# Kernel tuning notes

Measured on AMD Instinct MI355X. Metric: run time of the kernel, lower is better.

Reference implementation:

```python
import jax, jax.numpy as jnp
import numpy as np

H = 16        # num_heads
D_HEAD = 128  # head_dim
D = H * D_HEAD  # hidden_size = 2048


def setup_inputs() -> dict:
    key = jax.random.key(0)
    ks = jax.random.split(key, 9)
    s = 1.0 / np.sqrt(D)
    x = jax.random.normal(ks[0], (2, 2048, D), dtype=jnp.float32)
    Wq = jax.random.uniform(ks[1], (D, D), jnp.float32, -s, s)
    bq = jax.random.uniform(ks[2], (D,), jnp.float32, -s, s)
    Wk = jax.random.uniform(ks[3], (D, D), jnp.float32, -s, s)
    bk = jax.random.uniform(ks[4], (D,), jnp.float32, -s, s)
    Wv = jax.random.uniform(ks[5], (D, D), jnp.float32, -s, s)
    bv = jax.random.uniform(ks[6], (D,), jnp.float32, -s, s)
    Wo = jax.random.uniform(ks[7], (D, D), jnp.float32, -s, s)
    bo = jax.random.uniform(ks[8], (D,), jnp.float32, -s, s)
    return {"x": x, "Wq": Wq, "bq": bq, "Wk": Wk, "bk": bk,
            "Wv": Wv, "bv": bv, "Wo": Wo, "bo": bo}


def reference(x, Wq, bq, Wk, bk, Wv, bv, Wo, bo):
    B, T, _ = x.shape
    # Linear projections (torch Linear: x @ W.T + b)
    Q = x @ Wq.T + bq
    K = x @ Wk.T + bk
    V = x @ Wv.T + bv
    # [B, T, H, Dh] -> [B, H, T, Dh]
    Q = Q.reshape(B, T, H, D_HEAD).transpose(0, 2, 1, 3)
    K = K.reshape(B, T, H, D_HEAD).transpose(0, 2, 1, 3)
    V = V.reshape(B, T, H, D_HEAD).transpose(0, 2, 1, 3)
    scores = jnp.einsum('bhqd,bhkd->bhqk', Q, K) / jnp.sqrt(jnp.float32(D_HEAD))
    causal = jnp.tril(jnp.ones((T, T), dtype=bool))
    scores = jnp.where(causal, scores, -jnp.inf)
    probs = jax.nn.softmax(scores, axis=-1)
    ctx = jnp.einsum('bhqk,bhkd->bhqd', probs, V)  # [B, H, T, Dh]
    merged = ctx.transpose(0, 2, 1, 3).reshape(B, T, D)
    return merged @ Wo.T + bo
```

## Files before the change

### kernel.cpp

```cpp
#include <hip/hip_runtime.h>
#include <hip/hip_bf16.h>
#include <math.h>

typedef unsigned short ushort_t;
typedef short bf16x8 __attribute__((ext_vector_type(8)));
typedef float f32x4 __attribute__((ext_vector_type(4)));
typedef float f32x16 __attribute__((ext_vector_type(16)));

#define NH 16
#define DH 128
#define DM 2048
#define TSEQ 2048
#define BT 4096

__device__ __forceinline__ void async16(const void* g, void* l) {
  __builtin_amdgcn_global_load_lds(
      (const __attribute__((address_space(1))) void*)g,
      (__attribute__((address_space(3))) void*)l, 16, 0, 0);
}

__device__ __forceinline__ f32x4 mfma16(bf16x8 a, bf16x8 b, f32x4 c) {
  return __builtin_amdgcn_mfma_f32_16x16x32_bf16(a, b, c, 0, 0, 0);
}
__device__ __forceinline__ f32x16 mfma32(bf16x8 a, bf16x8 b, f32x16 c) {
  return __builtin_amdgcn_mfma_f32_32x32x16_bf16(a, b, c, 0, 0, 0);
}

__device__ __forceinline__ ushort_t f2bf(float f) {
  __hip_bfloat16 h = __float2bfloat16(f);
  return *reinterpret_cast<ushort_t*>(&h);
}
__device__ __forceinline__ unsigned cvtpk_bf16(float lo, float hi_) {
  unsigned r;
  asm("v_cvt_pk_bf16_f32 %0, %1, %2" : "=v"(r) : "v"(lo), "v"(hi_));
  return r;
}
__device__ __forceinline__ float fexp2(float x) {
  float r; asm("v_exp_f32 %0, %1" : "=v"(r) : "v"(x)); return r;
}

__global__ void cvt_kernel(const float* __restrict__ in, ushort_t* __restrict__ out, int n4) {
  const int i = blockIdx.x * blockDim.x + threadIdx.x;
  if (i >= n4) return;
  const float4 v = reinterpret_cast<const float4*>(in)[i];
  ushort4 u;
  u.x = f2bf(v.x); u.y = f2bf(v.y); u.z = f2bf(v.z); u.w = f2bf(v.w);
  reinterpret_cast<ushort4*>(out)[i] = u;
}

template<int MODE>
__global__ __launch_bounds__(256)
void gemm_kernel(const ushort_t* __restrict__ A,
                 const ushort_t* __restrict__ W_0, const ushort_t* __restrict__ W_1,
                 const ushort_t* __restrict__ W_2,
                 const float* __restrict__ b_0, const float* __restrict__ b_1,
                 const float* __restrict__ b_2,
                 ushort_t* __restrict__ outQ, ushort_t* __restrict__ outK,
                 ushort_t* __restrict__ outVt, float* __restrict__ outF)
{
  constexpr int K = DM;
  __shared__ __attribute__((aligned(16))) ushort_t As[128 * 64];
  __shared__ __attribute__((aligned(16))) ushort_t Bs[128 * 64];

  const int z = (MODE == 0) ? blockIdx.z : 0;
  const ushort_t* Wp = (MODE == 0) ? (z == 0 ? W_0 : (z == 1 ? W_1 : W_2)) : W_0;
  const float* bias  = (MODE == 0) ? (z == 0 ? b_0 : (z == 1 ? b_1 : b_2)) : b_0;

  const int n0 = blockIdx.x * 128;
  const int m0 = blockIdx.y * 128;
  const int tid = threadIdx.x;
  const int w = tid >> 6, l = tid & 63;
  const int wm = w >> 1, wn = w & 1;
  const int l15 = l & 15, l4 = l >> 4;

  f32x4 zero = {0.f, 0.f, 0.f, 0.f};
  f32x4 acc[4][4];
#pragma unroll
  for (int i = 0; i < 4; ++i)
#pragma unroll
    for (int j = 0; j < 4; ++j) acc[i][j] = zero;

  for (int k0 = 0; k0 < K; k0 += 64) {
    __syncthreads();
#pragma unroll
    for (int i = 0; i < 4; ++i) {
      const int rb = (i * 4 + w) * 8;
      const int r = rb + (l >> 3);
      const int c = ((l & 7) * 8) ^ ((r & 7) * 8);
      async16(A  + (size_t)(m0 + r) * K + k0 + c, &As[rb * 64]);
      async16(Wp + (size_t)(n0 + r) * K + k0 + c, &Bs[rb * 64]);
    }
    __syncthreads();
#pragma unroll
    for (int ks = 0; ks < 2; ++ks) {
      bf16x8 af[4], bfr[4];
#pragma unroll
      for (int mf = 0; mf < 4; ++mf) {
        const int row = wm * 64 + mf * 16 + l15;
        const int byte_ = row * 128 + ((l4 * 16 + ks * 64) ^ ((row & 7) << 4));
        af[mf] = *reinterpret_cast<const bf16x8*>(reinterpret_cast<const char*>(As) + byte_);
      }
#pragma unroll
      for (int nf = 0; nf < 4; ++nf) {
        const int row = wn * 64 + nf * 16 + l15;
        const int byte_ = row * 128 + ((l4 * 16 + ks * 64) ^ ((row & 7) << 4));
        bfr[nf] = *reinterpret_cast<const bf16x8*>(reinterpret_cast<const char*>(Bs) + byte_);
      }
#pragma unroll
      for (int mf = 0; mf < 4; ++mf)
#pragma unroll
        for (int nf = 0; nf < 4; ++nf)
          acc[mf][nf] = mfma16(af[mf], bfr[nf], acc[mf][nf]);
    }
  }

#pragma unroll
  for (int nf = 0; nf < 4; ++nf) {
    const int n = n0 + wn * 64 + nf * 16 + l15;
    const float bv = bias[n];
#pragma unroll
    for (int mf = 0; mf < 4; ++mf) {
#pragma unroll
      for (int r = 0; r < 4; ++r) {
        const int m = m0 + wm * 64 + mf * 16 + l4 * 4 + r;
        const float v = acc[mf][nf][r] + bv;
        if (MODE == 1) {
          outF[(size_t)m * DM + n] = v;
        } else {
          const int b = m >> 11, t = m & 2047;
          const int hh = n >> 7, d = n & 127;
          const ushort_t val = f2bf(v);
          if (z == 2) {
            outVt[((size_t)(b * NH + hh) * DH + d) * TSEQ + t] = val;
          } else {
            ushort_t* dst = (z == 0) ? outQ : outK;
            dst[((size_t)(b * NH + hh) * TSEQ + t) * DH + d] = val;
          }
        }
      }
    }
  }
}

__device__ __forceinline__ void stage_kv(const ushort_t* __restrict__ Kg,
                                         const ushort_t* __restrict__ Vt,
                                         size_t kbase, size_t vbase, int kv0,
                                         ushort_t* KsB, ushort_t* VsB, int tid)
{
#pragma unroll
  for (int i = 0; i < 4; ++i) {
    const int idx = i * 256 + tid;
    const int r = idx >> 4, ch = idx & 15;
    const int c = (ch ^ (r & 7)) * 8;
    async16(Kg + kbase + (size_t)(kv0 + r) * DH + c, KsB + idx * 8);
  }
#pragma unroll
  for (int i = 0; i < 4; ++i) {
    const int idx = i * 256 + tid;
    const int d = idx >> 3, ch = idx & 7;
    const int c = (ch ^ (d & 7)) * 8;
    async16(Vt + vbase + (size_t)d * TSEQ + kv0 + c, VsB + idx * 8);
  }
}

__global__ __launch_bounds__(256)
void attn_kernel(const ushort_t* __restrict__ Q, const ushort_t* __restrict__ Kg,
                 const ushort_t* __restrict__ Vt, ushort_t* __restrict__ ctx)
{
  __shared__ __attribute__((aligned(16))) ushort_t Ks[2][64 * 128];
  __shared__ __attribute__((aligned(16))) ushort_t Vs[2][128 * 64];

  const int fid = (int)blockIdx.x + 16 * (int)blockIdx.y;
  const int xcd = fid & 7;
  const int s   = fid >> 3;
  const int bh  = xcd * 4 + (s & 3);
  const int qt  = (s < 32) ? (15 - (s >> 2)) : ((s - 32) >> 2);

  const int tid = threadIdx.x, w = tid >> 6, l = tid & 63;
  const int l31 = l & 31, hi = l >> 5;
  const size_t kbase = (size_t)bh * TSEQ * DH;
  const size_t vbase = (size_t)bh * DH * TSEQ;
  const int bq0 = qt * 128;
  const int wq0 = bq0 + w * 32;
  const int NT = qt * 2 + 2;
  const int q = wq0 + l31;
  const float C2 = 0.12753842f;
  const float NEG = -3.0e38f;

  bf16x8 aq[8];
  {
    const ushort_t* qp = Q + kbase + (size_t)q * DH + hi * 8;
#pragma unroll
    for (int st = 0; st < 8; ++st)
      aq[st] = *reinterpret_cast<const bf16x8*>(qp + st * 16);
  }

  f32x16 o[4] = {};
  float m_r = NEG, l_r = 0.f;

  stage_kv(Kg, Vt, kbase, vbase, 0, Ks[0], Vs[0], tid);

  for (int kt = 0; kt < NT; ++kt) {
    const int kv0 = kt * 64, cur = kt & 1;
    if (kt + 1 < NT) {
      stage_kv(Kg, Vt, kbase, vbase, kv0 + 64, Ks[cur ^ 1], Vs[cur ^ 1], tid);
      asm volatile("s_waitcnt vmcnt(8)" ::: "memory");
    } else {
      asm volatile("s_waitcnt vmcnt(0)" ::: "memory");
    }
    __builtin_amdgcn_s_barrier();

    if (kv0 <= wq0 + 31) {
      const char* ksb = reinterpret_cast<const char*>(Ks[cur]);
      f32x16 s0 = {}, s1 = {};
      __builtin_amdgcn_s_setprio(1);
#pragma unroll
      for (int st = 0; st < 8; ++st) {
        const int byt = l31 * 256 + ((hi * 16 + st * 32) ^ ((l31 & 7) << 4));
        bf16x8 ak0 = *reinterpret_cast<const bf16x8*>(ksb + byt);
        bf16x8 ak1 = *reinterpret_cast<const bf16x8*>(ksb + byt + 8192);
        s0 = mfma32(ak0, aq[st], s0);
        s1 = mfma32(ak1, aq[st], s1);
      }
      __builtin_amdgcn_s_setprio(0);

      if (kv0 + 63 > wq0) {
#pragma unroll
        for (int r = 0; r < 16; ++r) {
          const int kvl = kv0 + (r & 3) + 8 * (r >> 2) + 4 * hi;
          if (kvl > q)      s0[r] = NEG;
          if (kvl + 32 > q) s1[r] = NEG;
        }
      }

      float t8[8];
#pragma unroll
      for (int r = 0; r < 8; ++r)
        t8[r] = fmaxf(fmaxf(s0[r], s0[r + 8]), fmaxf(s1[r], s1[r + 8]));
#pragma unroll
      for (int r = 0; r < 4; ++r) t8[r] = fmaxf(t8[r], t8[r + 4]);
      float mt = fmaxf(fmaxf(t8[0], t8[1]), fmaxf(t8[2], t8[3]));
      mt = fmaxf(mt, __shfl_xor(mt, 32));

      const float mnew = fmaxf(m_r, mt);
      if (!__all(mt <= m_r + 16.0f)) {
        const float alpha = fexp2((m_r - mnew) * C2);
        l_r *= alpha;
#pragma unroll
        for (int d0 = 0; d0 < 4; ++d0) o[d0] *= alpha;
        m_r = mnew;
      }

#pragma unroll
      for (int r = 0; r < 16; ++r) {
        s0[r] = fexp2((s0[r] - m_r) * C2);
        s1[r] = fexp2((s1[r] - m_r) * C2);
      }
      float sm[8];
#pragma unroll
      for (int r = 0; r < 8; ++r) sm[r] = (s0[r] + s0[r + 8]) + (s1[r] + s1[r + 8]);
#pragma unroll
      for (int r = 0; r < 4; ++r) sm[r] += sm[r + 4];
      float ls = (sm[0] + sm[1]) + (sm[2] + sm[3]);
      ls += __shfl_xor(ls, 32);
      l_r += ls;

      const char* vsb = reinterpret_cast<const char*>(Vs[cur]);
#pragma unroll
      for (int ks = 0; ks < 4; ++ks) {
        float pj[8];
#pragma unroll
        for (int j = 0; j < 8; ++j)
          pj[j] = (ks >> 1) ? s1[(ks & 1) * 8 + j] : s0[(ks & 1) * 8 + j];
        unsigned cA = cvtpk_bf16(pj[0], pj[1]);
        unsigned cB = cvtpk_bf16(pj[2], pj[3]);
        unsigned cC = cvtpk_bf16(pj[4], pj[5]);
        unsigned cD = cvtpk_bf16(pj[6], pj[7]);
        asm volatile("v_permlane32_swap_b32 %0, %1" : "+v"(cA), "+v"(cC));
        asm volatile("v_permlane32_swap_b32 %0, %1" : "+v"(cB), "+v"(cD));
        union { unsigned u[4]; bf16x8 v; } pa;
        pa.u[0] = cA; pa.u[1] = cB; pa.u[2] = cC; pa.u[3] = cD;
        __builtin_amdgcn_s_setprio(1);
#pragma unroll
        for (int d0 = 0; d0 < 4; ++d0) {
          const int byt = (d0 * 32 + l31) * 128 + ((ks * 32 + hi * 16) ^ ((l31 & 7) << 4));
          bf16x8 av = *reinterpret_cast<const bf16x8*>(vsb + byt);
          o[d0] = mfma32(av, pa.v, o[d0]);
        }
        __builtin_amdgcn_s_setprio(0);
      }
    }
    asm volatile("" ::: "memory");
    __builtin_amdgcn_s_barrier();
  }

  const size_t obase = (size_t)(bh >> 4) * TSEQ * DM + (size_t)(bh & 15) * DH;
  const float inv = 1.0f / l_r;
  ushort_t* cp = ctx + obase + (size_t)q * DM + hi * 4;
#pragma unroll
  for (int d0 = 0; d0 < 4; ++d0) {
#pragma unroll
    for (int g = 0; g < 4; ++g) {
      ushort4 u;
      u.x = f2bf(o[d0][4 * g + 0] * inv);
      u.y = f2bf(o[d0][4 * g + 1] * inv);
      u.z = f2bf(o[d0][4 * g + 2] * inv);
      u.w = f2bf(o[d0][4 * g + 3] * inv);
      *reinterpret_cast<ushort4*>(cp + d0 * 32 + 8 * g) = u;
    }
  }
}

extern "C" void kernel_launch(void* const* d_in, const int* in_sizes, int n_in,
                              void* d_out, int out_size, void* d_ws, size_t ws_size,
                              hipStream_t stream) {
  const float* x  = (const float*)d_in[0];
  const float* Wq = (const float*)d_in[1];
  const float* bq = (const float*)d_in[2];
  const float* Wk = (const float*)d_in[3];
  const float* bk = (const float*)d_in[4];
  const float* Wv = (const float*)d_in[5];
  const float* bv = (const float*)d_in[6];
  const float* Wo = (const float*)d_in[7];
  const float* bo = (const float*)d_in[8];
  float* out = (float*)d_out;

  char* ws = (char*)d_ws;
  ushort_t* xb  = (ushort_t*)ws;  ws += (size_t)BT * DM * 2;
  ushort_t* Wqb = (ushort_t*)ws;  ws += (size_t)DM * DM * 2;
  ushort_t* Wkb = (ushort_t*)ws;  ws += (size_t)DM * DM * 2;
  ushort_t* Wvb = (ushort_t*)ws;  ws += (size_t)DM * DM * 2;
  ushort_t* Wob = (ushort_t*)ws;  ws += (size_t)DM * DM * 2;
  ushort_t* Qb  = (ushort_t*)ws;  ws += (size_t)BT * DM * 2;
  ushort_t* Kb  = (ushort_t*)ws;  ws += (size_t)BT * DM * 2;
  ushort_t* Vtb = (ushort_t*)ws;  ws += (size_t)BT * DM * 2;
  ushort_t* ctxb = xb;

  const int nx4 = BT * DM / 4, nw4 = DM * DM / 4;
  cvt_kernel<<<nx4 / 256, 256, 0, stream>>>(x,  xb,  nx4);
  cvt_kernel<<<nw4 / 256, 256, 0, stream>>>(Wq, Wqb, nw4);
  cvt_kernel<<<nw4 / 256, 256, 0, stream>>>(Wk, Wkb, nw4);
  cvt_kernel<<<nw4 / 256, 256, 0, stream>>>(Wv, Wvb, nw4);
  cvt_kernel<<<nw4 / 256, 256, 0, stream>>>(Wo, Wob, nw4);

  gemm_kernel<0><<<dim3(DM / 128, BT / 128, 3), 256, 0, stream>>>(
      xb, Wqb, Wkb, Wvb, bq, bk, bv, Qb, Kb, Vtb, nullptr);

  attn_kernel<<<dim3(TSEQ / 128, 32), 256, 0, stream>>>(Qb, Kb, Vtb, ctxb);

  gemm_kernel<1><<<dim3(DM / 128, BT / 128, 1), 256, 0, stream>>>(
      ctxb, Wob, nullptr, nullptr, bo, nullptr, nullptr,
      nullptr, nullptr, nullptr, out);
}
```

Baseline: 298.9 us.

## Replace 128x128 GEMM with double-buffered 256x256 tiles and XCD-aware block mapping

The projection GEMMs move from 128x128 tiles with 4 waves and a single-buffered LDS stage to 256x256 tiles with 8 waves. K-tiles are double-buffered in four quarter stages, with explicit vmcnt waits and barriers so the next tile's global-to-LDS loads overlap MFMA work on the current one. Block indices are remapped so neighbouring tiles land on the same XCD to improve L2 reuse, and MFMA sections are wrapped in s_setprio. The cost is much larger LDS use (128KB per block), more register pressure, and fragile hand-tuned wait counts.

```diff
diff --git a/kernel.cpp b/kernel.cpp
--- a/kernel.cpp
+++ b/kernel.cpp
@@ -48,82 +48,145 @@
   reinterpret_cast<ushort4*>(out)[i] = u;
 }
 
+__device__ __forceinline__ void stage_half_g(const ushort_t* __restrict__ src,
+                                             int row0, int k0,
+                                             ushort_t* dst, int tid) {
+#pragma unroll
+  for (int i = 0; i < 2; ++i) {
+    const int idx = i * 512 + tid;
+    const int r = idx >> 3, ch = idx & 7;
+    const int c = (ch ^ (r & 7)) * 8;
+    async16(src + (size_t)(row0 + r) * DM + k0 + c, dst + idx * 8);
+  }
+}
+
 template<int MODE>
-__global__ __launch_bounds__(256)
-void gemm_kernel(const ushort_t* __restrict__ A,
-                 const ushort_t* __restrict__ W_0, const ushort_t* __restrict__ W_1,
-                 const ushort_t* __restrict__ W_2,
-                 const float* __restrict__ b_0, const float* __restrict__ b_1,
-                 const float* __restrict__ b_2,
-                 ushort_t* __restrict__ outQ, ushort_t* __restrict__ outK,
-                 ushort_t* __restrict__ outVt, float* __restrict__ outF)
+__global__ __launch_bounds__(512, 2)
+void gemm256_kernel(const ushort_t* __restrict__ A,
+                    const ushort_t* __restrict__ W_0, const ushort_t* __restrict__ W_1,
+                    const ushort_t* __restrict__ W_2,
+                    const float* __restrict__ b_0, const float* __restrict__ b_1,
+                    const float* __restrict__ b_2,
+                    ushort_t* __restrict__ outQ, ushort_t* __restrict__ outK,
+                    ushort_t* __restrict__ outVt, float* __restrict__ outF)
 {
-  constexpr int K = DM;
-  __shared__ __attribute__((aligned(16))) ushort_t As[128 * 64];
-  __shared__ __attribute__((aligned(16))) ushort_t Bs[128 * 64];
+  constexpr int NK = DM / 64;
+  __shared__ __attribute__((aligned(16))) ushort_t As[2][2][128 * 64];
+  __shared__ __attribute__((aligned(16))) ushort_t Bs[2][2][128 * 64];
 
   const int z = (MODE == 0) ? blockIdx.z : 0;
   const ushort_t* Wp = (MODE == 0) ? (z == 0 ? W_0 : (z == 1 ? W_1 : W_2)) : W_0;
   const float* bias  = (MODE == 0) ? (z == 0 ? b_0 : (z == 1 ? b_1 : b_2)) : b_0;
 
-  const int n0 = blockIdx.x * 128;
-  const int m0 = blockIdx.y * 128;
+  const int fid = (int)blockIdx.x + 8 * (int)blockIdx.y;
+  const int xcd = fid & 7, pos = fid >> 3;
+  const int n0 = ((xcd & 1) * 4 + (pos & 3)) * 256;
+  const int m0 = ((xcd >> 1) * 4 + (pos >> 2)) * 256;
+
   const int tid = threadIdx.x;
   const int w = tid >> 6, l = tid & 63;
-  const int wm = w >> 1, wn = w & 1;
+  const int wr = w >> 2, wc = w & 3;
   const int l15 = l & 15, l4 = l >> 4;
 
-  f32x4 zero = {0.f, 0.f, 0.f, 0.f};
-  f32x4 acc[4][4];
-#pragma unroll
-  for (int i = 0; i < 4; ++i)
-#pragma unroll
-    for (int j = 0; j < 4; ++j) acc[i][j] = zero;
-
-  for (int k0 = 0; k0 < K; k0 += 64) {
-    __syncthreads();
-#pragma unroll
-    for (int i = 0; i < 4; ++i) {
-      const int rb = (i * 4 + w) * 8;
-      const int r = rb + (l >> 3);
-      const int c = ((l & 7) * 8) ^ ((r & 7) * 8);
-      async16(A  + (size_t)(m0 + r) * K + k0 + c, &As[rb * 64]);
-      async16(Wp + (size_t)(n0 + r) * K + k0 + c, &Bs[rb * 64]);
-    }
-    __syncthreads();
-#pragma unroll
-    for (int ks = 0; ks < 2; ++ks) {
-      bf16x8 af[4], bfr[4];
-#pragma unroll
-      for (int mf = 0; mf < 4; ++mf) {
-        const int row = wm * 64 + mf * 16 + l15;
-        const int byte_ = row * 128 + ((l4 * 16 + ks * 64) ^ ((row & 7) << 4));
-        af[mf] = *reinterpret_cast<const bf16x8*>(reinterpret_cast<const char*>(As) + byte_);
-      }
-#pragma unroll
-      for (int nf = 0; nf < 4; ++nf) {
-        const int row = wn * 64 + nf * 16 + l15;
-        const int byte_ = row * 128 + ((l4 * 16 + ks * 64) ^ ((row & 7) << 4));
-        bfr[nf] = *reinterpret_cast<const bf16x8*>(reinterpret_cast<const char*>(Bs) + byte_);
-      }
-#pragma unroll
-      for (int mf = 0; mf < 4; ++mf)
-#pragma unroll
-        for (int nf = 0; nf < 4; ++nf)
-          acc[mf][nf] = mfma16(af[mf], bfr[nf], acc[mf][nf]);
-    }
-  }
-
-#pragma unroll
-  for (int nf = 0; nf < 4; ++nf) {
-    const int n = n0 + wn * 64 + nf * 16 + l15;
+  f32x4 acc[2][2][4][2] = {};
+  bf16x8 afr[4][2], bfr[2][2];
+
+#define LOAD_A(BUF, AH)                                                           \
+  { const char* p_ = reinterpret_cast<const char*>(As[BUF][AH]);                  \
+    _Pragma("unroll") for (int mf = 0; mf < 4; ++mf) {                            \
+      const int row_ = wr * 64 + mf * 16 + l15;                                   \
+      _Pragma("unroll") for (int ks = 0; ks < 2; ++ks)                            \
+        afr[mf][ks] = *reinterpret_cast<const bf16x8*>(                           \
+            p_ + row_ * 128 + ((l4 * 16 + ks * 64) ^ ((row_ & 7) << 4))); } }
+
+#define LOAD_B(BUF, BH)                                                           \
+  { const char* p_ = reinterpret_cast<const char*>(Bs[BUF][BH]);                  \
+    _Pragma("unroll") for (int nf = 0; nf < 2; ++nf) {                            \
+      const int row_ = wc * 32 + nf * 16 + l15;                                   \
+      _Pragma("unroll") for (int ks = 0; ks < 2; ++ks)                            \
+        bfr[nf][ks] = *reinterpret_cast<const bf16x8*>(                           \
+            p_ + row_ * 128 + ((l4 * 16 + ks * 64) ^ ((row_ & 7) << 4))); } }
+
+#define MM(AH, BH)                                                                \
+  __builtin_amdgcn_s_setprio(1);                                                  \
+  _Pragma("unroll") for (int mf = 0; mf < 4; ++mf)                                \
+  _Pragma("unroll") for (int nf = 0; nf < 2; ++nf)                                \
+  _Pragma("unroll") for (int ks = 0; ks < 2; ++ks)                                \
+    acc[AH][BH][mf][nf] = mfma16(afr[mf][ks], bfr[nf][ks], acc[AH][BH][mf][nf]);  \
+  __builtin_amdgcn_s_setprio(0);
+
+#define BARRIER() { asm volatile("" ::: "memory"); __builtin_amdgcn_s_barrier(); \
+                    asm volatile("" ::: "memory"); }
+
+  stage_half_g(A,  m0,       0, As[0][0], tid);
+  stage_half_g(Wp, n0,       0, Bs[0][0], tid);
+  stage_half_g(A,  m0 + 128, 0, As[0][1], tid);
+  stage_half_g(Wp, n0 + 128, 0, Bs[0][1], tid);
+
+  for (int kt = 0; kt < NK; ++kt) {
+    const int buf = kt & 1, nb = buf ^ 1;
+    const int k1 = (kt + 1) * 64;
+    const bool more = (kt + 1 < NK);
+
+    if (more) {
+      stage_half_g(A, m0, k1, As[nb][0], tid);
+      asm volatile("s_waitcnt vmcnt(6)" ::: "memory");
+    } else {
+      asm volatile("s_waitcnt vmcnt(4)" ::: "memory");
+    }
+    BARRIER();
+    LOAD_A(buf, 0); LOAD_B(buf, 0);
+    MM(0, 0);
+    BARRIER();
+
+    if (more) {
+      stage_half_g(Wp, n0, k1, Bs[nb][0], tid);
+      asm volatile("s_waitcnt vmcnt(6)" ::: "memory");
+    } else {
+      asm volatile("s_waitcnt vmcnt(2)" ::: "memory");
+    }
+    BARRIER();
+    LOAD_A(buf, 1);
+    MM(1, 0);
+    BARRIER();
+
+    if (more) {
+      stage_half_g(A, m0 + 128, k1, As[nb][1], tid);
+      asm volatile("s_waitcnt vmcnt(6)" ::: "memory");
+    } else {
+      asm volatile("s_waitcnt vmcnt(0)" ::: "memory");
+    }
+    BARRIER();
+    LOAD_B(buf, 1);
+    MM(1, 1);
+    BARRIER();
+
+    if (more) stage_half_g(Wp, n0 + 128, k1, Bs[nb][1], tid);
+    BARRIER();
+    LOAD_A(buf, 0);
+    MM(0, 1);
+    BARRIER();
+  }
+
+#undef LOAD_A
+#undef LOAD_B
+#undef MM
+#undef BARRIER
+
+#pragma unroll
+  for (int Ah = 0; Ah < 2; ++Ah)
+#pragma unroll
+  for (int Bh = 0; Bh < 2; ++Bh)
+#pragma unroll
+  for (int nf = 0; nf < 2; ++nf) {
+    const int n = n0 + Bh * 128 + wc * 32 + nf * 16 + l15;
     const float bv = bias[n];
 #pragma unroll
     for (int mf = 0; mf < 4; ++mf) {
 #pragma unroll
       for (int r = 0; r < 4; ++r) {
-        const int m = m0 + wm * 64 + mf * 16 + l4 * 4 + r;
-        const float v = acc[mf][nf][r] + bv;
+        const int m = m0 + Ah * 128 + wr * 64 + mf * 16 + l4 * 4 + r;
+        const float v = acc[Ah][Bh][mf][nf][r] + bv;
         if (MODE == 1) {
           outF[(size_t)m * DM + n] = v;
         } else {
@@ -343,12 +406,12 @@
   cvt_kernel<<<nw4 / 256, 256, 0, stream>>>(Wv, Wvb, nw4);
   cvt_kernel<<<nw4 / 256, 256, 0, stream>>>(Wo, Wob, nw4);
 
-  gemm_kernel<0><<<dim3(DM / 128, BT / 128, 3), 256, 0, stream>>>(
+  gemm256_kernel<0><<<dim3(8, 16, 3), 512, 0, stream>>>(
       xb, Wqb, Wkb, Wvb, bq, bk, bv, Qb, Kb, Vtb, nullptr);
 
   attn_kernel<<<dim3(TSEQ / 128, 32), 256, 0, stream>>>(Qb, Kb, Vtb, ctxb);
 
-  gemm_kernel<1><<<dim3(DM / 128, BT / 128, 1), 256, 0, stream>>>(
+  gemm256_kernel<1><<<dim3(8, 16, 1), 512, 0, stream>>>(
       ctxb, Wob, nullptr, nullptr, bo, nullptr, nullptr,
       nullptr, nullptr, nullptr, out);
 }
```

New measurement: 395.4 us. +32.3%, slower.
